# Kernel tuning notes

Hardware: AMD Instinct MI355X
Metric: run time of the kernel (lower is better)

Reference implementation:

```python
import jax, jax.numpy as jnp
import numpy as np
from jax import lax

B, T, IN_DIM, HIDDEN = 8, 4096, 1024, 1024


def setup_inputs() -> dict:
    key = jax.random.key(0)
    k_x, k_wd, k_wb = jax.random.split(key, 3)
    x = jax.random.normal(k_x, (B, T, IN_DIM), dtype=jnp.float32)
    h0 = jnp.zeros((B, HIDDEN), dtype=jnp.float32)
    # nn.Linear default init ~ U(-1/sqrt(in), 1/sqrt(in)); b_proj.weight ~ N(0, 0.02)
    lim = 1.0 / np.sqrt(IN_DIM)
    Wd = jax.random.uniform(k_wd, (HIDDEN, IN_DIM), jnp.float32, -lim, lim)
    bd = jnp.zeros((HIDDEN,), dtype=jnp.float32)
    Wb = 0.02 * jax.random.normal(k_wb, (HIDDEN, IN_DIM), dtype=jnp.float32)
    bb = jnp.zeros((HIDDEN,), dtype=jnp.float32)
    # 'hasani' init: A_log = log(linspace(0.5, 2.0, hidden))
    A_log = jnp.log(jnp.linspace(0.5, 2.0, HIDDEN, dtype=jnp.float32))
    return {"x": x, "h0": h0, "Wd": Wd, "bd": bd, "Wb": Wb, "bb": bb, "A_log": A_log}


def _combine(c1, c2):
    # composition of affine maps h -> a*h + b
    a1, b1 = c1
    a2, b2 = c2
    return a1 * a2, a2 * b1 + b2


def reference(x, h0, Wd, bd, Wb, bb, A_log):
    # projections: (B,T,in) @ (in,hidden)
    delta = jax.nn.softplus(jnp.einsum('bti,hi->bth', x, Wd) + bd)
    b_t = delta * (jnp.einsum('bti,hi->bth', x, Wb) + bb)
    A = jnp.exp(A_log)                      # (H,) decay rate
    A_t = jnp.exp(-delta * A)               # (B,T,H)
    # parallel (Blelloch/Heinsen-style) associative scan over T:
    # cumulative affine maps give h_t = A_cum_t * h0 + B_cum_t
    A_cum, B_cum = lax.associative_scan(_combine, (A_t, b_t), axis=1)
    h_full = A_cum * h0[:, None, :] + B_cum  # (B,T,H)
    return jnp.tanh(h_full)                  # bound=True
```

## Files before the change

kernel.cpp:

```cpp
#include <hip/hip_runtime.h>
#include <math.h>

#define B_DIM 8
#define T_DIM 4096
#define K_DIM 1024
#define H_DIM 1024
#define M_DIM (B_DIM * T_DIM)
#define BK 64
#define NTT 256

typedef short bf16x8 __attribute__((ext_vector_type(8)));
typedef float f32x4  __attribute__((ext_vector_type(4)));

__device__ __forceinline__ unsigned short f2bf(float f) {
  unsigned int u = __builtin_bit_cast(unsigned int, f);
  u += 0x7FFFu + ((u >> 16) & 1u);
  return (unsigned short)(u >> 16);
}

__device__ __forceinline__ void gload_lds16(const void* g, void* l) {
  __builtin_amdgcn_global_load_lds(
      (const __attribute__((address_space(1))) unsigned int*)g,
      (__attribute__((address_space(3))) unsigned int*)l,
      16 , 0 , 0 );
}

__device__ __forceinline__ float softplus_fast(float x) {
  float e = __expf(-fabsf(x));
  return fmaxf(x, 0.f) + __logf(1.f + e);
}

__device__ __forceinline__ float tanh_fast(float x) {
  float e = __expf(2.f * x);
  return 1.f - 2.f * __builtin_amdgcn_rcpf(e + 1.f);
}

__global__ __launch_bounds__(256) void k_cvt(const float* __restrict__ in,
                                             unsigned short* __restrict__ out,
                                             int n8) {
  int i = blockIdx.x * 256 + threadIdx.x;
  if (i >= n8) return;
  float4 v0 = ((const float4*)in)[i * 2 + 0];
  float4 v1 = ((const float4*)in)[i * 2 + 1];
  bf16x8 r;
  r[0] = (short)f2bf(v0.x); r[1] = (short)f2bf(v0.y);
  r[2] = (short)f2bf(v0.z); r[3] = (short)f2bf(v0.w);
  r[4] = (short)f2bf(v1.x); r[5] = (short)f2bf(v1.y);
  r[6] = (short)f2bf(v1.z); r[7] = (short)f2bf(v1.w);
  ((bf16x8*)out)[i] = r;
}

__global__ __launch_bounds__(256, 2) void k_mega(
    const unsigned short* __restrict__ Xb,
    const unsigned short* __restrict__ Wdb,
    const unsigned short* __restrict__ Wbb,
    const float* __restrict__ bd,
    const float* __restrict__ bb,
    const float* __restrict__ A_log,
    const float* __restrict__ h0,
    float* __restrict__ out)
{
  __shared__ unsigned short As[2][256 * BK];
  __shared__ unsigned short Bs[2][32 * BK];
  __shared__ float totA[4][16], totB[4][16];
  __shared__ float h_state[16];

  const int tid   = threadIdx.x;
  const int wg    = blockIdx.x;
  const int batch = wg & 7;
  const int jn    = wg >> 3;
  const int bn    = jn * 16;

  const int w    = tid >> 6;
  const int lane = tid & 63;
  const int c    = w;
  const int fr   = lane & 15;
  const int hi   = lane >> 4;
  const int gcol = bn + fr;

  const float bdv = bd[gcol];
  const float bbv = bb[gcol];
  const float Ah  = __expf(A_log[gcol]);

  const unsigned short* gA[8];
  int ldsA[8];
#pragma unroll
  for (int jj = 0; jj < 8; jj++) {
    int idx = jj * 256 + tid;
    int row = idx >> 3;
    int cg  = (idx & 7) ^ (row & 7);
    ldsA[jj] = idx * 16;
    gA[jj] = Xb + (((size_t)(batch * T_DIM + row)) << 10) + (size_t)(cg * 8);
  }
  const unsigned short* gB;
  int ldsB;
  {
    int idx = tid;
    int vr  = idx >> 3;
    int cg  = (idx & 7) ^ (vr & 7);
    ldsB = idx * 16;
    int h = bn + (vr & 15);
    const unsigned short* Wsrc = (vr & 16) ? Wbb : Wdb;
    gB = Wsrc + (((size_t)h) << 10) + (size_t)(cg * 8);
  }

  const int ch0 = hi ^ (fr & 7);
  const char* bA0 = (const char*)As + ((c * 64 + fr) * 128 + ch0 * 16);
  const char* bA1 = (const char*)As + ((c * 64 + fr) * 128 + (ch0 ^ 4) * 16);
  const char* bB0 = (const char*)Bs + (fr * 128 + ch0 * 16);
  const char* bB1 = (const char*)Bs + (fr * 128 + (ch0 ^ 4) * 16);

#define STAGE(TT, D)                                                          \
  do {                                                                        \
    int aOff = (((TT) >> 4) << 18) + (((TT) & 15) << 6);                      \
    int bOff = ((TT) & 15) << 6;                                              \
    _Pragma("unroll")                                                         \
    for (int jj = 0; jj < 8; jj++)                                            \
      gload_lds16(gA[jj] + aOff, (char*)As[D] + ldsA[jj]);                    \
    gload_lds16(gB + bOff, (char*)Bs[D] + ldsB);                              \
  } while (0)

#define TILE(TT, D)                                                           \
  do {                                                                        \
    if ((TT) < NTT - 1) STAGE((TT) + 1, (D) ^ 1);                             \
    bf16x8 Af[8], Bf[4];                                                      \
    _Pragma("unroll")                                                         \
    for (int mm = 0; mm < 4; mm++) {                                          \
      Af[mm * 2 + 0] = *(const bf16x8*)(bA0 + (D) * 32768 + mm * 2048);       \
      Af[mm * 2 + 1] = *(const bf16x8*)(bA1 + (D) * 32768 + mm * 2048);       \
    }                                                                         \
    _Pragma("unroll")                                                         \
    for (int nn = 0; nn < 2; nn++) {                                          \
      Bf[nn * 2 + 0] = *(const bf16x8*)(bB0 + (D) * 4096 + nn * 2048);        \
      Bf[nn * 2 + 1] = *(const bf16x8*)(bB1 + (D) * 4096 + nn * 2048);        \
    }                                                                         \
    __builtin_amdgcn_s_setprio(1);                                            \
    _Pragma("unroll")                                                         \
    for (int mm = 0; mm < 4; mm++)                                            \
      _Pragma("unroll")                                                       \
      for (int nn = 0; nn < 2; nn++)                                          \
        _Pragma("unroll")                                                     \
        for (int kk = 0; kk < 2; kk++)                                        \
          acc[mm][nn] = __builtin_amdgcn_mfma_f32_16x16x32_bf16(              \
              Af[mm * 2 + kk], Bf[nn * 2 + kk], acc[mm][nn], 0, 0, 0);        \
    __builtin_amdgcn_s_setprio(0);                                            \
    asm volatile("s_waitcnt vmcnt(0)" ::: "memory");                          \
    __builtin_amdgcn_s_barrier();                                             \
  } while (0)

  STAGE(0, 0);
  if (tid < 16) h_state[tid] = h0[(batch << 10) + bn + tid];
  asm volatile("s_waitcnt vmcnt(0)" ::: "memory");
  __syncthreads();

  const f32x4 z4 = {0.f, 0.f, 0.f, 0.f};

#pragma unroll 1
  for (int mt = 0; mt < 16; mt++) {
    f32x4 acc[4][2];
#pragma unroll
    for (int m = 0; m < 4; m++) { acc[m][0] = z4; acc[m][1] = z4; }

#pragma unroll 1
    for (int kp = 0; kp < 8; kp++) {
      int tt = mt * 16 + kp * 2;
      TILE(tt, 0);
      TILE(tt + 1, 1);
    }

    float rA[4], rB[4], wAp[4][4], wBp[4][4];
#pragma unroll
    for (int m = 0; m < 4; m++) {
      float A_ = 1.f, B_ = 0.f;
#pragma unroll
      for (int r = 0; r < 4; r++) {
        float z1  = acc[m][0][r] + bdv;
        float z2  = acc[m][1][r] + bbv;
        float dlt = softplus_fast(z1);
        float av  = __expf(-dlt * Ah);
        float bv  = dlt * z2;
        B_ = fmaf(av, B_, bv);
        A_ *= av;
        wAp[m][r] = A_; wBp[m][r] = B_;
      }
      rA[m] = A_; rB[m] = B_;
    }
    float cA = 1.f, cB = 0.f, eA[4], eB[4];
#pragma unroll
    for (int rho = 0; rho < 16; rho++) {
      if ((rho & 3) == hi) { eA[rho >> 2] = cA; eB[rho >> 2] = cB; }
      float sa = __shfl(rA[rho >> 2], (rho & 3) * 16 + fr, 64);
      float sb = __shfl(rB[rho >> 2], (rho & 3) * 16 + fr, 64);
      cB = fmaf(sa, cB, sb);
      cA *= sa;
    }
    if (hi == 0) { totA[c][fr] = cA; totB[c][fr] = cB; }
    __syncthreads();
    float hs = h_state[fr];
#pragma unroll
    for (int cc = 0; cc < 3; cc++) {
      float t2 = fmaf(totA[cc][fr], hs, totB[cc][fr]);
      hs = (cc < c) ? t2 : hs;
    }
    __syncthreads();
    if (c == 3 && hi == 0) h_state[fr] = fmaf(cA, hs, cB);

    size_t obase = (((size_t)(batch * T_DIM + mt * 256 + c * 64 + hi * 4)) << 10)
                   + (size_t)gcol;
#pragma unroll
    for (int m = 0; m < 4; m++) {
#pragma unroll
      for (int r = 0; r < 4; r++) {
        float aT = eA[m] * wAp[m][r];
        float bT = fmaf(wAp[m][r], eB[m], wBp[m][r]);
        float h  = fmaf(aT, hs, bT);
        out[obase + ((size_t)(m * 16 + r) << 10)] = tanh_fast(h);
      }
    }
  }
#undef TILE
#undef STAGE
}

extern "C" void kernel_launch(void* const* d_in, const int* in_sizes, int n_in,
                              void* d_out, int out_size, void* d_ws, size_t ws_size,
                              hipStream_t stream) {
  const float* x     = (const float*)d_in[0];
  const float* h0    = (const float*)d_in[1];
  const float* Wd    = (const float*)d_in[2];
  const float* bd    = (const float*)d_in[3];
  const float* Wb    = (const float*)d_in[4];
  const float* bb    = (const float*)d_in[5];
  const float* A_log = (const float*)d_in[6];
  float* out = (float*)d_out;

  char* ws = (char*)d_ws;
  unsigned short* xb  = (unsigned short*)(ws + 0);
  unsigned short* wdb = (unsigned short*)(ws + 67108864);
  unsigned short* wbb = (unsigned short*)(ws + 69206016);

  k_cvt<<<(M_DIM * K_DIM / 8) / 256, 256, 0, stream>>>(x, xb, M_DIM * K_DIM / 8);
  k_cvt<<<(H_DIM * K_DIM / 8) / 256, 256, 0, stream>>>(Wd, wdb, H_DIM * K_DIM / 8);
  k_cvt<<<(H_DIM * K_DIM / 8) / 256, 256, 0, stream>>>(Wb, wbb, H_DIM * K_DIM / 8);

  k_mega<<<512, 256, 0, stream>>>(xb, wdb, wbb, bd, bb, A_log, h0, out);
}
```

Baseline: 304.6 us.

## Split K across wave pairs in 512-thread blocks with LDS reduction

Doubles the threads per block and gives each pair of waves one 64-row chunk, with each wave handling half of the 64-wide K slice per tile. The partial accumulators are summed through LDS scratch before the scan epilogue, which only half the waves run. The aim is more waves per CU to hide load and MFMA latency, at the cost of an extra reduction, extra barriers, and redundant B-tile loads.

Result: slower. 380.2 us (+24.8%).

```diff
diff --git a/kernel.cpp b/kernel.cpp
--- a/kernel.cpp
+++ b/kernel.cpp
@@ -34,6 +34,13 @@
   float e = __expf(2.f * x);
   return 1.f - 2.f * __builtin_amdgcn_rcpf(e + 1.f);
 }
+
+#define LGKM_BAR()                                                            \
+  do {                                                                        \
+    asm volatile("s_waitcnt lgkmcnt(0)" ::: "memory");                        \
+    __builtin_amdgcn_sched_barrier(0);                                        \
+    __builtin_amdgcn_s_barrier();                                             \
+  } while (0)
 
 __global__ __launch_bounds__(256) void k_cvt(const float* __restrict__ in,
                                              unsigned short* __restrict__ out,
@@ -50,7 +57,7 @@
   ((bf16x8*)out)[i] = r;
 }
 
-__global__ __launch_bounds__(256, 2) void k_mega(
+__global__ __launch_bounds__(512, 4) void k_mega(
     const unsigned short* __restrict__ Xb,
     const unsigned short* __restrict__ Wdb,
     const unsigned short* __restrict__ Wbb,
@@ -73,7 +80,8 @@
 
   const int w    = tid >> 6;
   const int lane = tid & 63;
-  const int c    = w;
+  const int c    = w >> 1;
+  const int s    = w & 1;
   const int fr   = lane & 15;
   const int hi   = lane >> 4;
   const int gcol = bn + fr;
@@ -82,11 +90,11 @@
   const float bbv = bb[gcol];
   const float Ah  = __expf(A_log[gcol]);
 
-  const unsigned short* gA[8];
-  int ldsA[8];
-#pragma unroll
-  for (int jj = 0; jj < 8; jj++) {
-    int idx = jj * 256 + tid;
+  const unsigned short* gA[4];
+  int ldsA[4];
+#pragma unroll
+  for (int jj = 0; jj < 4; jj++) {
+    int idx = jj * 512 + tid;
     int row = idx >> 3;
     int cg  = (idx & 7) ^ (row & 7);
     ldsA[jj] = idx * 16;
@@ -95,54 +103,46 @@
   const unsigned short* gB;
   int ldsB;
   {
-    int idx = tid;
-    int vr  = idx >> 3;
-    int cg  = (idx & 7) ^ (vr & 7);
-    ldsB = idx * 16;
+    int t2  = tid & 255;
+    int vr  = t2 >> 3;
+    int cg  = (t2 & 7) ^ (vr & 7);
+    ldsB = t2 * 16;
     int h = bn + (vr & 15);
     const unsigned short* Wsrc = (vr & 16) ? Wbb : Wdb;
     gB = Wsrc + (((size_t)h) << 10) + (size_t)(cg * 8);
   }
 
-  const int ch0 = hi ^ (fr & 7);
-  const char* bA0 = (const char*)As + ((c * 64 + fr) * 128 + ch0 * 16);
-  const char* bA1 = (const char*)As + ((c * 64 + fr) * 128 + (ch0 ^ 4) * 16);
-  const char* bB0 = (const char*)Bs + (fr * 128 + ch0 * 16);
-  const char* bB1 = (const char*)Bs + (fr * 128 + (ch0 ^ 4) * 16);
+  const int ch0 = (s * 4 + hi) ^ (fr & 7);
+  const char* bA = (const char*)As + ((c * 64 + fr) * 128 + ch0 * 16);
+  const char* bB = (const char*)Bs + (fr * 128 + ch0 * 16);
 
 #define STAGE(TT, D)                                                          \
   do {                                                                        \
     int aOff = (((TT) >> 4) << 18) + (((TT) & 15) << 6);                      \
     int bOff = ((TT) & 15) << 6;                                              \
     _Pragma("unroll")                                                         \
-    for (int jj = 0; jj < 8; jj++)                                            \
+    for (int jj = 0; jj < 4; jj++)                                            \
       gload_lds16(gA[jj] + aOff, (char*)As[D] + ldsA[jj]);                    \
     gload_lds16(gB + bOff, (char*)Bs[D] + ldsB);                              \
   } while (0)
 
-#define TILE(TT, D)                                                           \
+#define BODY(TT, D)                                                           \
   do {                                                                        \
-    if ((TT) < NTT - 1) STAGE((TT) + 1, (D) ^ 1);                             \
-    bf16x8 Af[8], Bf[4];                                                      \
-    _Pragma("unroll")                                                         \
-    for (int mm = 0; mm < 4; mm++) {                                          \
-      Af[mm * 2 + 0] = *(const bf16x8*)(bA0 + (D) * 32768 + mm * 2048);       \
-      Af[mm * 2 + 1] = *(const bf16x8*)(bA1 + (D) * 32768 + mm * 2048);       \
-    }                                                                         \
-    _Pragma("unroll")                                                         \
-    for (int nn = 0; nn < 2; nn++) {                                          \
-      Bf[nn * 2 + 0] = *(const bf16x8*)(bB0 + (D) * 4096 + nn * 2048);        \
-      Bf[nn * 2 + 1] = *(const bf16x8*)(bB1 + (D) * 4096 + nn * 2048);        \
-    }                                                                         \
+    if ((TT) + 1 < NTT) STAGE((TT) + 1, (D) ^ 1);                             \
+    bf16x8 Af[4], Bf[2];                                                      \
+    _Pragma("unroll")                                                         \
+    for (int mm = 0; mm < 4; mm++)                                            \
+      Af[mm] = *(const bf16x8*)(bA + (D) * 32768 + mm * 2048);                \
+    _Pragma("unroll")                                                         \
+    for (int nn = 0; nn < 2; nn++)                                            \
+      Bf[nn] = *(const bf16x8*)(bB + (D) * 4096 + nn * 2048);                 \
     __builtin_amdgcn_s_setprio(1);                                            \
     _Pragma("unroll")                                                         \
     for (int mm = 0; mm < 4; mm++)                                            \
       _Pragma("unroll")                                                       \
       for (int nn = 0; nn < 2; nn++)                                          \
-        _Pragma("unroll")                                                     \
-        for (int kk = 0; kk < 2; kk++)                                        \
-          acc[mm][nn] = __builtin_amdgcn_mfma_f32_16x16x32_bf16(              \
-              Af[mm * 2 + kk], Bf[nn * 2 + kk], acc[mm][nn], 0, 0, 0);        \
+        acc[mm][nn] = __builtin_amdgcn_mfma_f32_16x16x32_bf16(                \
+            Af[mm], Bf[nn], acc[mm][nn], 0, 0, 0);                            \
     __builtin_amdgcn_s_setprio(0);                                            \
     asm volatile("s_waitcnt vmcnt(0)" ::: "memory");                          \
     __builtin_amdgcn_s_barrier();                                             \
@@ -151,9 +151,10 @@
   STAGE(0, 0);
   if (tid < 16) h_state[tid] = h0[(batch << 10) + bn + tid];
   asm volatile("s_waitcnt vmcnt(0)" ::: "memory");
-  __syncthreads();
+  __builtin_amdgcn_s_barrier();
 
   const f32x4 z4 = {0.f, 0.f, 0.f, 0.f};
+  char* scr = (char*)As[1] + c * 8192 + lane * 128;
 
 #pragma unroll 1
   for (int mt = 0; mt < 16; mt++) {
@@ -164,61 +165,85 @@
 #pragma unroll 1
     for (int kp = 0; kp < 8; kp++) {
       int tt = mt * 16 + kp * 2;
-      TILE(tt, 0);
-      TILE(tt + 1, 1);
-    }
-
-    float rA[4], rB[4], wAp[4][4], wBp[4][4];
-#pragma unroll
-    for (int m = 0; m < 4; m++) {
-      float A_ = 1.f, B_ = 0.f;
-#pragma unroll
-      for (int r = 0; r < 4; r++) {
-        float z1  = acc[m][0][r] + bdv;
-        float z2  = acc[m][1][r] + bbv;
-        float dlt = softplus_fast(z1);
-        float av  = __expf(-dlt * Ah);
-        float bv  = dlt * z2;
-        B_ = fmaf(av, B_, bv);
-        A_ *= av;
-        wAp[m][r] = A_; wBp[m][r] = B_;
-      }
-      rA[m] = A_; rB[m] = B_;
-    }
-    float cA = 1.f, cB = 0.f, eA[4], eB[4];
-#pragma unroll
-    for (int rho = 0; rho < 16; rho++) {
-      if ((rho & 3) == hi) { eA[rho >> 2] = cA; eB[rho >> 2] = cB; }
-      float sa = __shfl(rA[rho >> 2], (rho & 3) * 16 + fr, 64);
-      float sb = __shfl(rB[rho >> 2], (rho & 3) * 16 + fr, 64);
-      cB = fmaf(sa, cB, sb);
-      cA *= sa;
-    }
-    if (hi == 0) { totA[c][fr] = cA; totB[c][fr] = cB; }
-    __syncthreads();
-    float hs = h_state[fr];
-#pragma unroll
-    for (int cc = 0; cc < 3; cc++) {
-      float t2 = fmaf(totA[cc][fr], hs, totB[cc][fr]);
-      hs = (cc < c) ? t2 : hs;
-    }
-    __syncthreads();
-    if (c == 3 && hi == 0) h_state[fr] = fmaf(cA, hs, cB);
-
-    size_t obase = (((size_t)(batch * T_DIM + mt * 256 + c * 64 + hi * 4)) << 10)
-                   + (size_t)gcol;
-#pragma unroll
-    for (int m = 0; m < 4; m++) {
-#pragma unroll
-      for (int r = 0; r < 4; r++) {
-        float aT = eA[m] * wAp[m][r];
-        float bT = fmaf(wAp[m][r], eB[m], wBp[m][r]);
-        float h  = fmaf(aT, hs, bT);
-        out[obase + ((size_t)(m * 16 + r) << 10)] = tanh_fast(h);
+      BODY(tt, 0);
+      BODY(tt + 1, 1);
+    }
+
+    if (s == 1) {
+#pragma unroll
+      for (int m = 0; m < 4; m++)
+#pragma unroll
+        for (int n = 0; n < 2; n++)
+          *(f32x4*)(scr + (m * 2 + n) * 16) = acc[m][n];
+    }
+    LGKM_BAR();
+    if (s == 0) {
+#pragma unroll
+      for (int m = 0; m < 4; m++)
+#pragma unroll
+        for (int n = 0; n < 2; n++)
+          acc[m][n] += *(const f32x4*)(scr + (m * 2 + n) * 16);
+    }
+
+    float rA[4], rB[4], wAp[4][4], wBp[4][4], eA[4], eB[4];
+    float cA = 1.f, cB = 0.f;
+    if (s == 0) {
+#pragma unroll
+      for (int m = 0; m < 4; m++) {
+        float A_ = 1.f, B_ = 0.f;
+#pragma unroll
+        for (int r = 0; r < 4; r++) {
+          float z1  = acc[m][0][r] + bdv;
+          float z2  = acc[m][1][r] + bbv;
+          float dlt = softplus_fast(z1);
+          float av  = __expf(-dlt * Ah);
+          float bv  = dlt * z2;
+          B_ = fmaf(av, B_, bv);
+          A_ *= av;
+          wAp[m][r] = A_; wBp[m][r] = B_;
+        }
+        rA[m] = A_; rB[m] = B_;
+      }
+#pragma unroll
+      for (int rho = 0; rho < 16; rho++) {
+        if ((rho & 3) == hi) { eA[rho >> 2] = cA; eB[rho >> 2] = cB; }
+        float sa = __shfl(rA[rho >> 2], (rho & 3) * 16 + fr, 64);
+        float sb = __shfl(rB[rho >> 2], (rho & 3) * 16 + fr, 64);
+        cB = fmaf(sa, cB, sb);
+        cA *= sa;
+      }
+      if (hi == 0) { totA[c][fr] = cA; totB[c][fr] = cB; }
+    }
+    LGKM_BAR();
+    float hs = 0.f;
+    if (s == 0) {
+      hs = h_state[fr];
+#pragma unroll
+      for (int cc = 0; cc < 3; cc++) {
+        float t2 = fmaf(totA[cc][fr], hs, totB[cc][fr]);
+        hs = (cc < c) ? t2 : hs;
+      }
+    }
+    LGKM_BAR();
+    if (s == 0 && c == 3 && hi == 0) h_state[fr] = fmaf(cA, hs, cB);
+
+    if (s == 0) {
+      size_t obase =
+          (((size_t)(batch * T_DIM + mt * 256 + c * 64 + hi * 4)) << 10)
+          + (size_t)gcol;
+#pragma unroll
+      for (int m = 0; m < 4; m++) {
+#pragma unroll
+        for (int r = 0; r < 4; r++) {
+          float aT = eA[m] * wAp[m][r];
+          float bT = fmaf(wAp[m][r], eB[m], wBp[m][r]);
+          float h  = fmaf(aT, hs, bT);
+          out[obase + ((size_t)(m * 16 + r) << 10)] = tanh_fast(h);
+        }
       }
     }
   }
-#undef TILE
+#undef BODY
 #undef STAGE
 }
 
@@ -243,5 +268,5 @@
   k_cvt<<<(H_DIM * K_DIM / 8) / 256, 256, 0, stream>>>(Wd, wdb, H_DIM * K_DIM / 8);
   k_cvt<<<(H_DIM * K_DIM / 8) / 256, 256, 0, stream>>>(Wb, wbb, H_DIM * K_DIM / 8);
 
-  k_mega<<<512, 256, 0, stream>>>(xb, wdb, wbb, bd, bb, A_log, h0, out);
-}
+  k_mega<<<512, 512, 0, stream>>>(xb, wdb, wbb, bd, bb, A_log, h0, out);
+}
```

## Split time dimension across workgroups with decoupled lookback chained scan

Applied to the files above, without the earlier changes.

Instead of 512 workgroups each looping over 16 time tiles sequentially, launch 8192 workgroups, one per (batch, column block, time segment). Each computes its GEMM tile and local scan independently, then waits on a flag from the previous segment to get its carry-in hidden state and publishes its own end state. This exposes more parallelism and removes the per-WG serial loop. The risk is spin-wait latency along a 16-long chain, and a possible deadlock if a later segment is scheduled before its predecessor, since block-ID ordering is relied on.

Result: slower. 1.028 ms (+237.6%).

```diff
diff --git a/kernel.cpp b/kernel.cpp
--- a/kernel.cpp
+++ b/kernel.cpp
@@ -7,7 +7,9 @@
 #define H_DIM 1024
 #define M_DIM (B_DIM * T_DIM)
 #define BK 64
-#define NTT 256
+#define NKT 16
+#define NSEG 16
+#define NCHAIN 512
 
 typedef short bf16x8 __attribute__((ext_vector_type(8)));
 typedef float f32x4  __attribute__((ext_vector_type(4)));
@@ -50,6 +52,10 @@
   ((bf16x8*)out)[i] = r;
 }
 
+__global__ __launch_bounds__(256) void k_clear(unsigned int* __restrict__ f) {
+  f[blockIdx.x * 256 + threadIdx.x] = 0u;
+}
+
 __global__ __launch_bounds__(256, 2) void k_mega(
     const unsigned short* __restrict__ Xb,
     const unsigned short* __restrict__ Wdb,
@@ -58,18 +64,22 @@
     const float* __restrict__ bb,
     const float* __restrict__ A_log,
     const float* __restrict__ h0,
+    float* __restrict__ chainh,
+    unsigned int* __restrict__ flags,
     float* __restrict__ out)
 {
   __shared__ unsigned short As[2][256 * BK];
   __shared__ unsigned short Bs[2][32 * BK];
   __shared__ float totA[4][16], totB[4][16];
-  __shared__ float h_state[16];
+  __shared__ float hs_sh[16];
 
   const int tid   = threadIdx.x;
-  const int wg    = blockIdx.x;
-  const int batch = wg & 7;
-  const int jn    = wg >> 3;
-  const int bn    = jn * 16;
+  const int wgid  = blockIdx.x;
+  const int batch = wgid & 7;
+  const int col   = (wgid >> 3) & 63;
+  const int seg   = wgid >> 9;
+  const int bn    = col * 16;
+  const int fcid  = (batch * 64 + col) * NSEG;
 
   const int w    = tid >> 6;
   const int lane = tid & 63;
@@ -90,7 +100,8 @@
     int row = idx >> 3;
     int cg  = (idx & 7) ^ (row & 7);
     ldsA[jj] = idx * 16;
-    gA[jj] = Xb + (((size_t)(batch * T_DIM + row)) << 10) + (size_t)(cg * 8);
+    gA[jj] = Xb + (((size_t)(batch * T_DIM + seg * 256 + row)) << 10)
+                + (size_t)(cg * 8);
   }
   const unsigned short* gB;
   int ldsB;
@@ -112,17 +123,16 @@
 
 #define STAGE(TT, D)                                                          \
   do {                                                                        \
-    int aOff = (((TT) >> 4) << 18) + (((TT) & 15) << 6);                      \
-    int bOff = ((TT) & 15) << 6;                                              \
+    int kOff = (TT) << 6;                                                     \
     _Pragma("unroll")                                                         \
     for (int jj = 0; jj < 8; jj++)                                            \
-      gload_lds16(gA[jj] + aOff, (char*)As[D] + ldsA[jj]);                    \
-    gload_lds16(gB + bOff, (char*)Bs[D] + ldsB);                              \
+      gload_lds16(gA[jj] + kOff, (char*)As[D] + ldsA[jj]);                    \
+    gload_lds16(gB + kOff, (char*)Bs[D] + ldsB);                              \
   } while (0)
 
 #define TILE(TT, D)                                                           \
   do {                                                                        \
-    if ((TT) < NTT - 1) STAGE((TT) + 1, (D) ^ 1);                             \
+    if ((TT) < NKT - 1) STAGE((TT) + 1, (D) ^ 1);                             \
     bf16x8 Af[8], Bf[4];                                                      \
     _Pragma("unroll")                                                         \
     for (int mm = 0; mm < 4; mm++) {                                          \
@@ -149,73 +159,85 @@
   } while (0)
 
   STAGE(0, 0);
-  if (tid < 16) h_state[tid] = h0[(batch << 10) + bn + tid];
   asm volatile("s_waitcnt vmcnt(0)" ::: "memory");
+  __builtin_amdgcn_s_barrier();
+
+  const f32x4 z4 = {0.f, 0.f, 0.f, 0.f};
+  f32x4 acc[4][2];
+#pragma unroll
+  for (int m = 0; m < 4; m++) { acc[m][0] = z4; acc[m][1] = z4; }
+
+#pragma unroll 1
+  for (int kp = 0; kp < 8; kp++) {
+    TILE(kp * 2, 0);
+    TILE(kp * 2 + 1, 1);
+  }
+
+  float rA[4], rB[4], wAp[4][4], wBp[4][4];
+#pragma unroll
+  for (int m = 0; m < 4; m++) {
+    float A_ = 1.f, B_ = 0.f;
+#pragma unroll
+    for (int r = 0; r < 4; r++) {
+      float z1  = acc[m][0][r] + bdv;
+      float z2  = acc[m][1][r] + bbv;
+      float dlt = softplus_fast(z1);
+      float av  = __expf(-dlt * Ah);
+      float bv  = dlt * z2;
+      B_ = fmaf(av, B_, bv);
+      A_ *= av;
+      wAp[m][r] = A_; wBp[m][r] = B_;
+    }
+    rA[m] = A_; rB[m] = B_;
+  }
+  float cA = 1.f, cB = 0.f, eA[4], eB[4];
+#pragma unroll
+  for (int rho = 0; rho < 16; rho++) {
+    if ((rho & 3) == hi) { eA[rho >> 2] = cA; eB[rho >> 2] = cB; }
+    float sa = __shfl(rA[rho >> 2], (rho & 3) * 16 + fr, 64);
+    float sb = __shfl(rB[rho >> 2], (rho & 3) * 16 + fr, 64);
+    cB = fmaf(sa, cB, sb);
+    cA *= sa;
+  }
+  if (hi == 0) { totA[c][fr] = cA; totB[c][fr] = cB; }
   __syncthreads();
 
-  const f32x4 z4 = {0.f, 0.f, 0.f, 0.f};
-
-#pragma unroll 1
-  for (int mt = 0; mt < 16; mt++) {
-    f32x4 acc[4][2];
-#pragma unroll
-    for (int m = 0; m < 4; m++) { acc[m][0] = z4; acc[m][1] = z4; }
-
-#pragma unroll 1
-    for (int kp = 0; kp < 8; kp++) {
-      int tt = mt * 16 + kp * 2;
-      TILE(tt, 0);
-      TILE(tt + 1, 1);
-    }
-
-    float rA[4], rB[4], wAp[4][4], wBp[4][4];
-#pragma unroll
-    for (int m = 0; m < 4; m++) {
-      float A_ = 1.f, B_ = 0.f;
-#pragma unroll
-      for (int r = 0; r < 4; r++) {
-        float z1  = acc[m][0][r] + bdv;
-        float z2  = acc[m][1][r] + bbv;
-        float dlt = softplus_fast(z1);
-        float av  = __expf(-dlt * Ah);
-        float bv  = dlt * z2;
-        B_ = fmaf(av, B_, bv);
-        A_ *= av;
-        wAp[m][r] = A_; wBp[m][r] = B_;
-      }
-      rA[m] = A_; rB[m] = B_;
-    }
-    float cA = 1.f, cB = 0.f, eA[4], eB[4];
-#pragma unroll
-    for (int rho = 0; rho < 16; rho++) {
-      if ((rho & 3) == hi) { eA[rho >> 2] = cA; eB[rho >> 2] = cB; }
-      float sa = __shfl(rA[rho >> 2], (rho & 3) * 16 + fr, 64);
-      float sb = __shfl(rB[rho >> 2], (rho & 3) * 16 + fr, 64);
-      cB = fmaf(sa, cB, sb);
-      cA *= sa;
-    }
-    if (hi == 0) { totA[c][fr] = cA; totB[c][fr] = cB; }
-    __syncthreads();
-    float hs = h_state[fr];
-#pragma unroll
-    for (int cc = 0; cc < 3; cc++) {
-      float t2 = fmaf(totA[cc][fr], hs, totB[cc][fr]);
-      hs = (cc < c) ? t2 : hs;
-    }
-    __syncthreads();
-    if (c == 3 && hi == 0) h_state[fr] = fmaf(cA, hs, cB);
-
-    size_t obase = (((size_t)(batch * T_DIM + mt * 256 + c * 64 + hi * 4)) << 10)
-                   + (size_t)gcol;
-#pragma unroll
-    for (int m = 0; m < 4; m++) {
-#pragma unroll
-      for (int r = 0; r < 4; r++) {
-        float aT = eA[m] * wAp[m][r];
-        float bT = fmaf(wAp[m][r], eB[m], wBp[m][r]);
-        float h  = fmaf(aT, hs, bT);
-        out[obase + ((size_t)(m * 16 + r) << 10)] = tanh_fast(h);
-      }
+  if (seg != 0 && tid == 0) {
+    while (atomicOr(&flags[fcid + seg - 1], 0u) == 0u)
+      __builtin_amdgcn_s_sleep(2);
+  }
+  __syncthreads();
+  __threadfence();
+  if (tid < 16)
+    hs_sh[tid] = (seg == 0) ? h0[(batch << 10) + bn + tid]
+                            : chainh[(size_t)(fcid + seg - 1) * 16 + tid];
+  __syncthreads();
+
+  float hs = hs_sh[fr];
+#pragma unroll
+  for (int cc = 0; cc < 3; cc++) {
+    float t2 = fmaf(totA[cc][fr], hs, totB[cc][fr]);
+    hs = (cc < c) ? t2 : hs;
+  }
+
+  if (c == 3) {
+    float hend = fmaf(cA, hs, cB);
+    if (lane < 16) chainh[(size_t)(fcid + seg) * 16 + fr] = hend;
+    __threadfence();
+    if (lane == 0) atomicExch(&flags[fcid + seg], 1u);
+  }
+
+  size_t obase =
+      (((size_t)(batch * T_DIM + seg * 256 + c * 64 + hi * 4)) << 10)
+      + (size_t)gcol;
+#pragma unroll
+  for (int m = 0; m < 4; m++) {
+#pragma unroll
+    for (int r = 0; r < 4; r++) {
+      float aT = eA[m] * wAp[m][r];
+      float bT = fmaf(wAp[m][r], eB[m], wBp[m][r]);
+      float h  = fmaf(aT, hs, bT);
+      out[obase + ((size_t)(m * 16 + r) << 10)] = tanh_fast(h);
     }
   }
 #undef TILE
@@ -235,13 +257,17 @@
   float* out = (float*)d_out;
 
   char* ws = (char*)d_ws;
-  unsigned short* xb  = (unsigned short*)(ws + 0);
-  unsigned short* wdb = (unsigned short*)(ws + 67108864);
-  unsigned short* wbb = (unsigned short*)(ws + 69206016);
+  unsigned short* xb     = (unsigned short*)(ws + 0);
+  unsigned short* wdb    = (unsigned short*)(ws + 67108864);
+  unsigned short* wbb    = (unsigned short*)(ws + 69206016);
+  float*          chainh = (float*)(ws + 71303168);
+  unsigned int*   flags  = (unsigned int*)(ws + 71827456);
 
   k_cvt<<<(M_DIM * K_DIM / 8) / 256, 256, 0, stream>>>(x, xb, M_DIM * K_DIM / 8);
   k_cvt<<<(H_DIM * K_DIM / 8) / 256, 256, 0, stream>>>(Wd, wdb, H_DIM * K_DIM / 8);
   k_cvt<<<(H_DIM * K_DIM / 8) / 256, 256, 0, stream>>>(Wb, wbb, H_DIM * K_DIM / 8);
-
-  k_mega<<<512, 256, 0, stream>>>(xb, wdb, wbb, bd, bb, A_log, h0, out);
-}
+  k_clear<<<(NCHAIN * NSEG) / 256, 256, 0, stream>>>(flags);
+
+  k_mega<<<NCHAIN * NSEG, 256, 0, stream>>>(xb, wdb, wbb, bd, bb, A_log, h0,
+                                            chainh, flags, out);
+}
```

## Keep weight slice resident in LDS and stream X fragments directly to registers

Applied to the files above, without the earlier changes.

Loads the block's full 32x1024 bf16 weight slice (Wd and Wb rows) into LDS once at kernel start, instead of staging a small B tile per k-step. X fragments are read straight from global memory into registers with double-buffered prefetch, which removes the A-tile LDS staging and the per-tile barriers and vmcnt waits. This relies on the cache hierarchy to absorb the uncoalesced per-lane 16-byte global loads of X. It also makes each wave fetch its own rows directly, which could expose global latency if prefetch depth is insufficient, and it raises register pressure.

Result: slower. 508.0 us (+66.8%).

```diff
diff --git a/kernel.cpp b/kernel.cpp
--- a/kernel.cpp
+++ b/kernel.cpp
@@ -6,8 +6,6 @@
 #define K_DIM 1024
 #define H_DIM 1024
 #define M_DIM (B_DIM * T_DIM)
-#define BK 64
-#define NTT 256
 
 typedef short bf16x8 __attribute__((ext_vector_type(8)));
 typedef float f32x4  __attribute__((ext_vector_type(4)));
@@ -21,8 +19,7 @@
 __device__ __forceinline__ void gload_lds16(const void* g, void* l) {
   __builtin_amdgcn_global_load_lds(
       (const __attribute__((address_space(1))) unsigned int*)g,
-      (__attribute__((address_space(3))) unsigned int*)l,
-      16 , 0 , 0 );
+      (__attribute__((address_space(3))) unsigned int*)l, 16, 0, 0);
 }
 
 __device__ __forceinline__ float softplus_fast(float x) {
@@ -60,20 +57,17 @@
     const float* __restrict__ h0,
     float* __restrict__ out)
 {
-  __shared__ unsigned short As[2][256 * BK];
-  __shared__ unsigned short Bs[2][32 * BK];
+  __shared__ unsigned short Bs[32 * 1024];
   __shared__ float totA[4][16], totB[4][16];
   __shared__ float h_state[16];
 
   const int tid   = threadIdx.x;
   const int wg    = blockIdx.x;
   const int batch = wg & 7;
-  const int jn    = wg >> 3;
-  const int bn    = jn * 16;
-
-  const int w    = tid >> 6;
+  const int bn    = (wg >> 3) * 16;
+
+  const int c    = tid >> 6;
   const int lane = tid & 63;
-  const int c    = w;
   const int fr   = lane & 15;
   const int hi   = lane >> 4;
   const int gcol = bn + fr;
@@ -82,78 +76,57 @@
   const float bbv = bb[gcol];
   const float Ah  = __expf(A_log[gcol]);
 
-  const unsigned short* gA[8];
-  int ldsA[8];
-#pragma unroll
-  for (int jj = 0; jj < 8; jj++) {
+#pragma unroll
+  for (int jj = 0; jj < 16; jj++) {
     int idx = jj * 256 + tid;
-    int row = idx >> 3;
-    int cg  = (idx & 7) ^ (row & 7);
-    ldsA[jj] = idx * 16;
-    gA[jj] = Xb + (((size_t)(batch * T_DIM + row)) << 10) + (size_t)(cg * 8);
+    int v   = idx >> 7;
+    int cc  = idx & 127;
+    int cs  = cc ^ (v & 7);
+    const unsigned short* Wsrc = (v & 16) ? Wbb : Wdb;
+    gload_lds16(Wsrc + (((size_t)(bn + (v & 15))) << 10) + (size_t)(cs * 8),
+                (char*)Bs + idx * 16);
   }
-  const unsigned short* gB;
-  int ldsB;
-  {
-    int idx = tid;
-    int vr  = idx >> 3;
-    int cg  = (idx & 7) ^ (vr & 7);
-    ldsB = idx * 16;
-    int h = bn + (vr & 15);
-    const unsigned short* Wsrc = (vr & 16) ? Wbb : Wdb;
-    gB = Wsrc + (((size_t)h) << 10) + (size_t)(cg * 8);
-  }
-
-  const int ch0 = hi ^ (fr & 7);
-  const char* bA0 = (const char*)As + ((c * 64 + fr) * 128 + ch0 * 16);
-  const char* bA1 = (const char*)As + ((c * 64 + fr) * 128 + (ch0 ^ 4) * 16);
-  const char* bB0 = (const char*)Bs + (fr * 128 + ch0 * 16);
-  const char* bB1 = (const char*)Bs + (fr * 128 + (ch0 ^ 4) * 16);
-
-#define STAGE(TT, D)                                                          \
-  do {                                                                        \
-    int aOff = (((TT) >> 4) << 18) + (((TT) & 15) << 6);                      \
-    int bOff = ((TT) & 15) << 6;                                              \
-    _Pragma("unroll")                                                         \
-    for (int jj = 0; jj < 8; jj++)                                            \
-      gload_lds16(gA[jj] + aOff, (char*)As[D] + ldsA[jj]);                    \
-    gload_lds16(gB + bOff, (char*)Bs[D] + ldsB);                              \
-  } while (0)
-
-#define TILE(TT, D)                                                           \
-  do {                                                                        \
-    if ((TT) < NTT - 1) STAGE((TT) + 1, (D) ^ 1);                             \
-    bf16x8 Af[8], Bf[4];                                                      \
-    _Pragma("unroll")                                                         \
-    for (int mm = 0; mm < 4; mm++) {                                          \
-      Af[mm * 2 + 0] = *(const bf16x8*)(bA0 + (D) * 32768 + mm * 2048);       \
-      Af[mm * 2 + 1] = *(const bf16x8*)(bA1 + (D) * 32768 + mm * 2048);       \
-    }                                                                         \
-    _Pragma("unroll")                                                         \
-    for (int nn = 0; nn < 2; nn++) {                                          \
-      Bf[nn * 2 + 0] = *(const bf16x8*)(bB0 + (D) * 4096 + nn * 2048);        \
-      Bf[nn * 2 + 1] = *(const bf16x8*)(bB1 + (D) * 4096 + nn * 2048);        \
-    }                                                                         \
-    __builtin_amdgcn_s_setprio(1);                                            \
-    _Pragma("unroll")                                                         \
-    for (int mm = 0; mm < 4; mm++)                                            \
-      _Pragma("unroll")                                                       \
-      for (int nn = 0; nn < 2; nn++)                                          \
-        _Pragma("unroll")                                                     \
-        for (int kk = 0; kk < 2; kk++)                                        \
-          acc[mm][nn] = __builtin_amdgcn_mfma_f32_16x16x32_bf16(              \
-              Af[mm * 2 + kk], Bf[nn * 2 + kk], acc[mm][nn], 0, 0, 0);        \
-    __builtin_amdgcn_s_setprio(0);                                            \
-    asm volatile("s_waitcnt vmcnt(0)" ::: "memory");                          \
-    __builtin_amdgcn_s_barrier();                                             \
-  } while (0)
-
-  STAGE(0, 0);
   if (tid < 16) h_state[tid] = h0[(batch << 10) + bn + tid];
   asm volatile("s_waitcnt vmcnt(0)" ::: "memory");
   __syncthreads();
 
+  const unsigned short* pA =
+      Xb + (((size_t)(batch * T_DIM + c * 64 + fr)) << 10) + (size_t)(hi * 8);
+
+  const char* bB = (const char*)Bs + fr * 2048;
+  const int   sw = fr & 7;
+
   const f32x4 z4 = {0.f, 0.f, 0.f, 0.f};
+
+  bf16x8 aP[4], aQ[4], bP[2], bQ[2];
+
+#define PF_A(SET, PM, KS)                                                     \
+  do {                                                                        \
+    SET[0] = *(const bf16x8*)((PM) + 0 * 16384 + (KS) * 32);                  \
+    SET[1] = *(const bf16x8*)((PM) + 1 * 16384 + (KS) * 32);                  \
+    SET[2] = *(const bf16x8*)((PM) + 2 * 16384 + (KS) * 32);                  \
+    SET[3] = *(const bf16x8*)((PM) + 3 * 16384 + (KS) * 32);                  \
+  } while (0)
+#define PF_B(SET, KS)                                                         \
+  do {                                                                        \
+    int ch = (((KS) * 4 + hi) ^ sw) * 16;                                     \
+    SET[0] = *(const bf16x8*)(bB + ch);                                       \
+    SET[1] = *(const bf16x8*)(bB + 32768 + ch);                               \
+  } while (0)
+#define MFMA8(ASET, BSET)                                                     \
+  do {                                                                        \
+    _Pragma("unroll")                                                         \
+    for (int mm = 0; mm < 4; mm++) {                                          \
+      acc[mm][0] = __builtin_amdgcn_mfma_f32_16x16x32_bf16(                   \
+          ASET[mm], BSET[0], acc[mm][0], 0, 0, 0);                            \
+      acc[mm][1] = __builtin_amdgcn_mfma_f32_16x16x32_bf16(                   \
+          ASET[mm], BSET[1], acc[mm][1], 0, 0, 0);                            \
+    }                                                                         \
+  } while (0)
+
+  const unsigned short* pm = pA;
+  PF_A(aP, pm, 0);
+  PF_B(bP, 0);
 
 #pragma unroll 1
   for (int mt = 0; mt < 16; mt++) {
@@ -161,11 +134,22 @@
 #pragma unroll
     for (int m = 0; m < 4; m++) { acc[m][0] = z4; acc[m][1] = z4; }
 
-#pragma unroll 1
-    for (int kp = 0; kp < 8; kp++) {
-      int tt = mt * 16 + kp * 2;
-      TILE(tt, 0);
-      TILE(tt + 1, 1);
+#pragma unroll
+    for (int ks = 0; ks < 32; ks++) {
+      if (ks & 1) {
+        if (ks < 31) {
+          PF_A(aP, pm, ks + 1);
+          PF_B(bP, ks + 1);
+        } else {
+          pm += 262144;
+          if (mt < 15) { PF_A(aP, pm, 0); PF_B(bP, 0); }
+        }
+        MFMA8(aQ, bQ);
+      } else {
+        PF_A(aQ, pm, ks + 1);
+        PF_B(bQ, ks + 1);
+        MFMA8(aP, bP);
+      }
     }
 
     float rA[4], rB[4], wAp[4][4], wBp[4][4];
@@ -205,8 +189,9 @@
     __syncthreads();
     if (c == 3 && hi == 0) h_state[fr] = fmaf(cA, hs, cB);
 
-    size_t obase = (((size_t)(batch * T_DIM + mt * 256 + c * 64 + hi * 4)) << 10)
-                   + (size_t)gcol;
+    size_t obase =
+        (((size_t)(batch * T_DIM + mt * 256 + c * 64 + hi * 4)) << 10)
+        + (size_t)gcol;
 #pragma unroll
     for (int m = 0; m < 4; m++) {
 #pragma unroll
@@ -218,8 +203,9 @@
       }
     }
   }
-#undef TILE
-#undef STAGE
+#undef PF_A
+#undef PF_B
+#undef MFMA8
 }
 
 extern "C" void kernel_launch(void* const* d_in, const int* in_sizes, int n_in,
```
